# Kernel tuning notes

Hardware: AMD Instinct MI355X
Metric: run time of the kernel (lower is better)

Reference implementation:

```python
import jax, jax.numpy as jnp
import numpy as np

VOCAB, D, S, T, B, E, C = 21128, 768, 50, 5, 512, 128, 10


def gcn(x, edges, W, b):
    # GCNConv with self-loops and symmetric normalization. x: [S, D]
    N = x.shape[0]
    loop = jnp.arange(N)
    src = jnp.concatenate([edges[0], loop])
    dst = jnp.concatenate([edges[1], loop])
    deg = jax.ops.segment_sum(jnp.ones_like(src, dtype=x.dtype), dst, num_segments=N)
    dinv = jax.lax.rsqrt(jnp.maximum(deg, 1e-12))
    norm = dinv[src] * dinv[dst]
    h = x @ W  # [S, 10]
    out = jax.ops.segment_sum(h[src] * norm[:, None], dst, num_segments=N)
    return out + b


def mpm(self_f, cross_f, assign, W1, b1, W2, b2):
    # multi-perspective matching, broadcast over leading dims; node dim = -2
    a = assign * self_f
    c = assign * cross_f
    num = jnp.sum(a * c, axis=-1)
    den = jnp.maximum(jnp.linalg.norm(a, axis=-1) * jnp.linalg.norm(c, axis=-1), 1e-8)
    cos = num / den
    bshape = jnp.broadcast_shapes(self_f.shape[:-2], cross_f.shape[:-2])
    sf = jnp.broadcast_to(self_f, bshape + self_f.shape[-2:])
    h = jnp.concatenate([cos[..., None], sf], axis=-1)  # [..., S, 11]
    h = jax.nn.relu(h @ W1 + b1) @ W2 + b2  # [..., S, 20]
    return jnp.max(h, axis=-2)  # [..., 20]


def setup_inputs() -> dict:
    key = jax.random.key(0)
    ks = jax.random.split(key, 20)
    inp = {
        "context_input": jax.random.randint(ks[0], (B, T, S), 0, VOCAB),
        "response_input": jax.random.randint(ks[1], (B, S), 0, VOCAB),
        "context_graph_adjs": jax.random.randint(ks[2], (B, T, 2, E), 0, S),
        "response_graph_adj": jax.random.randint(ks[3], (B, 2, E), 0, S),
        "word_emb": jax.random.normal(ks[4], (VOCAB, D), jnp.float32) * 0.02,
        "conv_W": jax.random.normal(ks[5], (D, C), jnp.float32) * 0.05,
        "conv_b": jnp.zeros((C,), jnp.float32),
        "cross_w": jax.random.uniform(ks[6], (D, C), jnp.float32),
        "attention_coef": jax.random.uniform(ks[7], (S, S), jnp.float32),
        "assign_weight": jax.random.uniform(ks[8], (S, C), jnp.float32),
        "mp_W1": jax.random.normal(ks[9], (C + 1, 20), jnp.float32) * 0.3,
        "mp_b1": jnp.zeros((20,), jnp.float32),
        "mp_W2": jax.random.normal(ks[10], (20, 20), jnp.float32) * 0.2,
        "mp_b2": jnp.zeros((20,), jnp.float32),
        "ffn_W1": jax.random.normal(ks[11], (80, 40), jnp.float32) * 0.1,
        "ffn_b1": jnp.zeros((40,), jnp.float32),
        "ffn_W2": jax.random.normal(ks[12], (40, 1), jnp.float32) * 0.2,
        "ffn_b2": jnp.zeros((1,), jnp.float32),
    }
    return inp


def reference(context_input, response_input, context_graph_adjs, response_graph_adj,
              word_emb, conv_W, conv_b, cross_w, attention_coef, assign_weight,
              mp_W1, mp_b1, mp_W2, mp_b2, ffn_W1, ffn_b1, ffn_W2, ffn_b2):
    ctx = word_emb[context_input]      # [B, T, S, D]
    resp = word_emb[response_input]    # [B, S, D]

    gcn_b = jax.vmap(gcn, in_axes=(0, 0, None, None))
    resp_gcn = gcn_b(resp, response_graph_adj, conv_W, conv_b)                      # [B, S, C]
    ctx_gcn = jax.vmap(gcn_b, in_axes=(0, 0, None, None))(ctx, context_graph_adjs, conv_W, conv_b)  # [B, T, S, C]

    # cross features: utterance cross comes from response, response cross from utterance
    u_cross = jnp.einsum('ps,bsk->bpk', attention_coef, resp @ cross_w)   # [B, S, C]
    r_cross = jnp.einsum('ps,btsk->btpk', attention_coef, ctx @ cross_w)  # [B, T, S, C]

    g_u = mpm(ctx_gcn, u_cross[:, None], assign_weight, mp_W1, mp_b1, mp_W2, mp_b2)       # [B, T, 20]
    g_r = mpm(resp_gcn[:, None], r_cross, assign_weight, mp_W1, mp_b1, mp_W2, mp_b2)      # [B, T, 20]

    feat = jnp.concatenate([g_u, g_r, g_u * g_r, jnp.abs(g_u - g_r)], axis=-1)  # [B, T, 80]
    logits = jax.nn.relu(feat @ ffn_W1 + ffn_b1) @ ffn_W2 + ffn_b2              # [B, T, 1]
    return jax.nn.sigmoid(jnp.sum(logits, axis=1))                              # [B, 1]
```

## Files before the change

kernel.cpp:

```cpp
#include <hip/hip_runtime.h>
#include <math.h>

#define VOCAB 21128
#define DD 768
#define SS 50
#define TT 5
#define BB 512
#define EE 128
#define CC 10
#define V20 (VOCAB * 20)
#define NG 2560
#define NALL 3072

__global__ __launch_bounds__(512) void k_vocab(const float* __restrict__ emb,
                                               const float* __restrict__ Wconv,
                                               const float* __restrict__ Wcross,
                                               const float* __restrict__ att,
                                               float* __restrict__ attG,
                                               float* __restrict__ hvp) {
    __shared__ float tile[8][64][21];
    const int wv = threadIdx.x >> 6, lane = threadIdx.x & 63;
    const int rowbase = blockIdx.x * 64;

    if (rowbase >= VOCAB) {
        if (blockIdx.y == 0) {
            for (int i = threadIdx.x; i < SS * SS; i += 512) {
                int p = i / SS, s = i - p * SS;
                attG[s * 52 + p] = att[i];
            }
        }
        return;
    }

    const int rsub = lane >> 2, m = lane & 3;
    const int d0w = blockIdx.y * 384 + __builtin_amdgcn_readfirstlane(wv * 48);

    float4 v[12];
#pragma unroll
    for (int ch = 0; ch < 3; ++ch) {
#pragma unroll
        for (int it = 0; it < 4; ++it) {
            int row = it * 16 + rsub;
            long r = rowbase + row;
            if (r >= VOCAB) r = VOCAB - 1;
            v[ch * 4 + it] = *(const float4*)(emb + r * DD + d0w + ch * 16 + m * 4);
        }
    }

    float acc[20];
#pragma unroll
    for (int c = 0; c < 20; c++) acc[c] = 0.f;

#pragma unroll
    for (int ch = 0; ch < 3; ++ch) {
        const int d0 = d0w + ch * 16;
#pragma unroll
        for (int it = 0; it < 4; ++it) {
            const int row = it * 16 + rsub;
            const float4 w = v[ch * 4 + it];
            tile[wv][row][m * 4 + 0] = w.x;
            tile[wv][row][m * 4 + 1] = w.y;
            tile[wv][row][m * 4 + 2] = w.z;
            tile[wv][row][m * 4 + 3] = w.w;
        }
#pragma unroll
        for (int d = 0; d < 16; ++d) {
            float e = tile[wv][lane][d];
            const float* wc = Wconv + (d0 + d) * 10;
            const float* wx = Wcross + (d0 + d) * 10;
#pragma unroll
            for (int c = 0; c < 10; c++) {
                acc[c] = fmaf(e, wc[c], acc[c]);
                acc[10 + c] = fmaf(e, wx[c], acc[10 + c]);
            }
        }
    }

    __syncthreads();
    float* pp = &tile[0][0][0];
#pragma unroll
    for (int c = 0; c < 20; c++) pp[wv * 1280 + lane * 20 + c] = acc[c];
    __syncthreads();
    float* outp = hvp + (long)blockIdx.y * V20;
    for (int i = threadIdx.x; i < 1280; i += 512) {
        int row = i / 20;
        long r = rowbase + row;
        if (r < VOCAB) {
            float s = 0.f;
#pragma unroll
            for (int w = 0; w < 8; ++w) s += pp[w * 1280 + i];
            outp[r * 20 + (i - row * 20)] = s;
        }
    }
}

__global__ __launch_bounds__(256) void k_gcn(const int* __restrict__ ctok,
                                             const int* __restrict__ cadj,
                                             const int* __restrict__ rtok,
                                             const int* __restrict__ radj,
                                             const float* __restrict__ hvp,
                                             const float* __restrict__ convb,
                                             const float* __restrict__ attG,
                                             float* __restrict__ P) {
    __shared__ float hcv[4][SS][12];
    __shared__ float aggL[4][SS][11];
    __shared__ int dgS[4][64];
    const int tid = threadIdx.x, wv = tid >> 6, lane = tid & 63;
    const int G = blockIdx.x * 4 + wv;

    const int* tb;
    const int* ab;
    if (G < NG) { tb = ctok + (long)G * SS; ab = cadj + (long)G * 2 * EE; }
    else        { int b = G - NG; tb = rtok + (long)b * SS; ab = radj + (long)b * 2 * EE; }

    const int e1s = ab[lane], e2s = ab[lane + 64];
    const int e1d = ab[EE + lane], e2d = ab[EE + lane + 64];

    const int p = lane;
    const int pc = (p < SS) ? p : (SS - 1);
    const long t = tb[pc];
    const float4* hv4 = (const float4*)hvp;

    float4 qa[5], qb[5];
#pragma unroll
    for (int qi = 0; qi < 5; ++qi) {
        qa[qi] = hv4[t * 5 + qi];
        qb[qi] = hv4[(long)(VOCAB * 5) + t * 5 + qi];
    }
    float rowv[CC], xo[CC];
    rowv[0] = qa[0].x + qb[0].x; rowv[1] = qa[0].y + qb[0].y;
    rowv[2] = qa[0].z + qb[0].z; rowv[3] = qa[0].w + qb[0].w;
    rowv[4] = qa[1].x + qb[1].x; rowv[5] = qa[1].y + qb[1].y;
    rowv[6] = qa[1].z + qb[1].z; rowv[7] = qa[1].w + qb[1].w;
    rowv[8] = qa[2].x + qb[2].x; rowv[9] = qa[2].y + qb[2].y;
    xo[0] = qa[2].z + qb[2].z; xo[1] = qa[2].w + qb[2].w;
    xo[2] = qa[3].x + qb[3].x; xo[3] = qa[3].y + qb[3].y;
    xo[4] = qa[3].z + qb[3].z; xo[5] = qa[3].w + qb[3].w;
    xo[6] = qa[4].x + qb[4].x; xo[7] = qa[4].y + qb[4].y;
    xo[8] = qa[4].z + qb[4].z; xo[9] = qa[4].w + qb[4].w;

    dgS[wv][lane] = 0;
    atomicAdd(&dgS[wv][e1d], 1);
    atomicAdd(&dgS[wv][e2d], 1);

    if (p < SS) {
        *(float4*)&hcv[wv][p][0] = make_float4(rowv[0], rowv[1], rowv[2], rowv[3]);
        *(float4*)&hcv[wv][p][4] = make_float4(rowv[4], rowv[5], rowv[6], rowv[7]);
        *(float2*)&hcv[wv][p][8] = make_float2(rowv[8], rowv[9]);
    }

    float dv = 0.f;
    if (lane < SS) dv = rsqrtf((float)(dgS[wv][lane] + 1));

    float* aggW = &aggL[wv][0][0];
    for (int i = lane; i < SS * 11; i += 64) aggW[i] = 0.f;
    const float n1 = __shfl(dv, e1s) * __shfl(dv, e1d);
    const float n2 = __shfl(dv, e2s) * __shfl(dv, e2d);
#pragma unroll
    for (int c = 0; c < CC; c++) atomicAdd(&aggW[e1d * 11 + c], hcv[wv][e1s][c] * n1);
#pragma unroll
    for (int c = 0; c < CC; c++) atomicAdd(&aggW[e2d * 11 + c], hcv[wv][e2s][c] * n2);

    if (p < SS) {
        float gcn[CC];
        const float dp2 = dv * dv;
#pragma unroll
        for (int c = 0; c < CC; c++) gcn[c] = aggW[p * 11 + c] + rowv[c] * dp2 + convb[c];

        float ax[CC];
#pragma unroll
        for (int c = 0; c < CC; c++) ax[c] = 0.f;
#pragma unroll 5
        for (int s = 0; s < SS; ++s) {
            const float a = attG[s * 52 + p];
#pragma unroll
            for (int c = 0; c < CC; c++) {
                const float xs = __uint_as_float(
                    __builtin_amdgcn_readlane(__float_as_uint(xo[c]), s));
                ax[c] = fmaf(a, xs, ax[c]);
            }
        }
        float4* o4 = (float4*)(P + (long)G * 1000 + p * 20);
        o4[0] = make_float4(gcn[0], gcn[1], gcn[2], gcn[3]);
        o4[1] = make_float4(gcn[4], gcn[5], gcn[6], gcn[7]);
        o4[2] = make_float4(gcn[8], gcn[9], ax[0], ax[1]);
        o4[3] = make_float4(ax[2], ax[3], ax[4], ax[5]);
        o4[4] = make_float4(ax[6], ax[7], ax[8], ax[9]);
    }
}

__global__ __launch_bounds__(640) void k_mpmf(const float* __restrict__ P,
                                              const float* __restrict__ assign,
                                              const float* __restrict__ W1, const float* __restrict__ b1,
                                              const float* __restrict__ W2, const float* __restrict__ b2,
                                              const float* __restrict__ fW1, const float* __restrict__ fb1,
                                              const float* __restrict__ fW2, const float* __restrict__ fb2,
                                              float* __restrict__ out) {
    __shared__ float W2T[20][21];
    __shared__ float asgL[SS][11];
    __shared__ float h1L[10][SS][20];
    __shared__ float guS[TT][20];
    __shared__ float grS[TT][20];
    __shared__ float fsum[256];
    const int tid = threadIdx.x, wv = tid >> 6, lane = tid & 63;
    const int b = blockIdx.x;
    const int t = wv >> 1, which = wv & 1;
    const int g = b * TT + t;

    for (int i = tid; i < 400; i += 640) W2T[i % 20][i / 20] = W2[i];
    for (int i = tid; i < SS * CC; i += 640) asgL[i / CC][i % CC] = assign[i];
    __syncthreads();

    const float* Pc = P + (long)g * 1000;
    const float* Pr = P + (long)(NG + b) * 1000;
    const float* selfP = which ? Pr : Pc;
    const float* croP  = which ? Pc : Pr;

    const int p = lane;
    float self[CC], cro[CC];
    if (p < SS) {
        const float4* s4 = (const float4*)(selfP + p * 20);
        const float4 a0 = s4[0], a1 = s4[1], a2 = s4[2];
        self[0] = a0.x; self[1] = a0.y; self[2] = a0.z; self[3] = a0.w;
        self[4] = a1.x; self[5] = a1.y; self[6] = a1.z; self[7] = a1.w;
        self[8] = a2.x; self[9] = a2.y;
        const float4* c4 = (const float4*)(croP + p * 20);
        const float4 b0 = c4[2], b1q = c4[3], b2q = c4[4];
        cro[0] = b0.z; cro[1] = b0.w;
        cro[2] = b1q.x; cro[3] = b1q.y; cro[4] = b1q.z; cro[5] = b1q.w;
        cro[6] = b2q.x; cro[7] = b2q.y; cro[8] = b2q.z; cro[9] = b2q.w;
    }

    const int j = lane % 20;
    const int grp = lane / 20;
    float w2r[20];
#pragma unroll
    for (int k = 0; k < 20; k++) w2r[k] = W2T[j][k];

    if (p < SS) {
        float num = 0.f, na = 0.f, nc2 = 0.f;
#pragma unroll
        for (int c = 0; c < CC; c++) {
            float av = asgL[p][c];
            float a = av * self[c];
            float cx = av * cro[c];
            num = fmaf(a, cx, num);
            na = fmaf(a, a, na);
            nc2 = fmaf(cx, cx, nc2);
        }
        float cosv = num / fmaxf(sqrtf(na) * sqrtf(nc2), 1e-8f);
        float h1[20];
#pragma unroll
        for (int q = 0; q < 20; q++) h1[q] = fmaf(cosv, W1[q], b1[q]);
#pragma unroll
        for (int k = 0; k < CC; k++) {
            float sv = self[k];
#pragma unroll
            for (int q = 0; q < 20; q++) h1[q] = fmaf(sv, W1[(k + 1) * 20 + q], h1[q]);
        }
        float4* hw = (float4*)&h1L[wv][p][0];
        hw[0] = make_float4(fmaxf(h1[0], 0.f), fmaxf(h1[1], 0.f), fmaxf(h1[2], 0.f), fmaxf(h1[3], 0.f));
        hw[1] = make_float4(fmaxf(h1[4], 0.f), fmaxf(h1[5], 0.f), fmaxf(h1[6], 0.f), fmaxf(h1[7], 0.f));
        hw[2] = make_float4(fmaxf(h1[8], 0.f), fmaxf(h1[9], 0.f), fmaxf(h1[10], 0.f), fmaxf(h1[11], 0.f));
        hw[3] = make_float4(fmaxf(h1[12], 0.f), fmaxf(h1[13], 0.f), fmaxf(h1[14], 0.f), fmaxf(h1[15], 0.f));
        hw[4] = make_float4(fmaxf(h1[16], 0.f), fmaxf(h1[17], 0.f), fmaxf(h1[18], 0.f), fmaxf(h1[19], 0.f));
    }

    float part = -1e30f;
    if (grp < 3) {
        const int s0 = grp * 17;
        const int s1 = (grp == 2) ? SS : (s0 + 17);
        for (int s = s0; s < s1; ++s) {
            const float* hr = &h1L[wv][s][0];
            float tt = 0.f;
#pragma unroll
            for (int k = 0; k < 20; k++) tt = fmaf(hr[k], w2r[k], tt);
            part = fmaxf(part, tt);
        }
    }
    const float a0 = __shfl(part, j);
    const float a1 = __shfl(part, j + 20);
    const float a2 = __shfl(part, j + 40);
    if (lane < 20) {
        float h2 = fmaxf(fmaxf(a0, a1), a2) + b2[lane];
        (which ? grS[t] : guS[t])[lane] = h2;
    }
    __syncthreads();

    float term = 0.f;
    if (tid < 200) {
        const int tt = tid / 40, jj = tid - tt * 40;
        float hvv = fb1[jj];
#pragma unroll
        for (int k = 0; k < 20; k++) {
            float u = guS[tt][k], r = grS[tt][k];
            hvv = fmaf(u, fW1[k * 40 + jj], hvv);
            hvv = fmaf(r, fW1[(20 + k) * 40 + jj], hvv);
            hvv = fmaf(u * r, fW1[(40 + k) * 40 + jj], hvv);
            hvv = fmaf(fabsf(u - r), fW1[(60 + k) * 40 + jj], hvv);
        }
        term = fmaxf(hvv, 0.f) * fW2[jj];
    }
    if (tid < 256) fsum[tid] = term;
    __syncthreads();
    if (wv == 0) {
        float s = fsum[lane] + fsum[lane + 64] + fsum[lane + 128] + fsum[lane + 192];
#pragma unroll
        for (int o = 32; o; o >>= 1) s += __shfl_xor(s, o);
        if (lane == 0) out[b] = 1.f / (1.f + expf(-(s + (float)TT * fb2[0])));
    }
}

extern "C" void kernel_launch(void* const* d_in, const int* in_sizes, int n_in,
                              void* d_out, int out_size, void* d_ws, size_t ws_size,
                              hipStream_t stream) {
    (void)in_sizes; (void)n_in; (void)out_size; (void)ws_size;
    const int* ctx_tok = (const int*)d_in[0];
    const int* resp_tok = (const int*)d_in[1];
    const int* ctx_adj = (const int*)d_in[2];
    const int* resp_adj = (const int*)d_in[3];
    const float* emb = (const float*)d_in[4];
    const float* convW = (const float*)d_in[5];
    const float* convb = (const float*)d_in[6];
    const float* crossW = (const float*)d_in[7];
    const float* att = (const float*)d_in[8];
    const float* assign = (const float*)d_in[9];
    const float* mpW1 = (const float*)d_in[10];
    const float* mpb1 = (const float*)d_in[11];
    const float* mpW2 = (const float*)d_in[12];
    const float* mpb2 = (const float*)d_in[13];
    const float* fW1 = (const float*)d_in[14];
    const float* fb1 = (const float*)d_in[15];
    const float* fW2 = (const float*)d_in[16];
    const float* fb2 = (const float*)d_in[17];

    float* ws = (float*)d_ws;
    float* hvp = ws;
    float* P = hvp + 2 * V20;
    float* attG = P + (long)NALL * 1000;
    float* outf = (float*)d_out;

    hipLaunchKernelGGL(k_vocab, dim3((VOCAB + 63) / 64 + 1, 2), dim3(512), 0, stream,
                       emb, convW, crossW, att, attG, hvp);
    hipLaunchKernelGGL(k_gcn, dim3(NALL / 4), dim3(256), 0, stream,
                       ctx_tok, ctx_adj, resp_tok, resp_adj, hvp, convb, attG, P);
    hipLaunchKernelGGL(k_mpmf, dim3(BB), dim3(640), 0, stream,
                       P, assign, mpW1, mpb1, mpW2, mpb2, fW1, fb1, fW2, fb2, outf);
}
```

Measured before the change: 69.60 us.

## Fuse GCN and matching kernels into one per-batch kernel with LDS handoff

Merges the GCN/cross-attention kernel into the matching+FFN kernel so each block computes the six graphs of one batch (5 contexts + response) in waves 0-5 and passes them through shared memory. This removes the global round-trip of the P buffer and one kernel launch, and avoids recomputing nothing extra since the response graph is now computed once per batch. It also replaces the LDS-staged second MLP layer with per-lane register accumulation and a wave-wide shuffle max reduction. In exchange, only 6 of 10 waves do GCN work before a barrier, and the per-lane 20x20 register matmul raises register pressure.

```diff
diff --git a/kernel.cpp b/kernel.cpp
--- a/kernel.cpp
+++ b/kernel.cpp
@@ -10,7 +10,6 @@
 #define CC 10
 #define V20 (VOCAB * 20)
 #define NG 2560
-#define NALL 3072
 
 __global__ __launch_bounds__(512) void k_vocab(const float* __restrict__ emb,
                                                const float* __restrict__ Wconv,
@@ -94,154 +93,128 @@
     }
 }
 
-__global__ __launch_bounds__(256) void k_gcn(const int* __restrict__ ctok,
-                                             const int* __restrict__ cadj,
-                                             const int* __restrict__ rtok,
-                                             const int* __restrict__ radj,
-                                             const float* __restrict__ hvp,
-                                             const float* __restrict__ convb,
-                                             const float* __restrict__ attG,
-                                             float* __restrict__ P) {
-    __shared__ float hcv[4][SS][12];
-    __shared__ float aggL[4][SS][11];
-    __shared__ int dgS[4][64];
-    const int tid = threadIdx.x, wv = tid >> 6, lane = tid & 63;
-    const int G = blockIdx.x * 4 + wv;
-
-    const int* tb;
-    const int* ab;
-    if (G < NG) { tb = ctok + (long)G * SS; ab = cadj + (long)G * 2 * EE; }
-    else        { int b = G - NG; tb = rtok + (long)b * SS; ab = radj + (long)b * 2 * EE; }
-
-    const int e1s = ab[lane], e2s = ab[lane + 64];
-    const int e1d = ab[EE + lane], e2d = ab[EE + lane + 64];
-
-    const int p = lane;
-    const int pc = (p < SS) ? p : (SS - 1);
-    const long t = tb[pc];
-    const float4* hv4 = (const float4*)hvp;
-
-    float4 qa[5], qb[5];
-#pragma unroll
-    for (int qi = 0; qi < 5; ++qi) {
-        qa[qi] = hv4[t * 5 + qi];
-        qb[qi] = hv4[(long)(VOCAB * 5) + t * 5 + qi];
-    }
-    float rowv[CC], xo[CC];
-    rowv[0] = qa[0].x + qb[0].x; rowv[1] = qa[0].y + qb[0].y;
-    rowv[2] = qa[0].z + qb[0].z; rowv[3] = qa[0].w + qb[0].w;
-    rowv[4] = qa[1].x + qb[1].x; rowv[5] = qa[1].y + qb[1].y;
-    rowv[6] = qa[1].z + qb[1].z; rowv[7] = qa[1].w + qb[1].w;
-    rowv[8] = qa[2].x + qb[2].x; rowv[9] = qa[2].y + qb[2].y;
-    xo[0] = qa[2].z + qb[2].z; xo[1] = qa[2].w + qb[2].w;
-    xo[2] = qa[3].x + qb[3].x; xo[3] = qa[3].y + qb[3].y;
-    xo[4] = qa[3].z + qb[3].z; xo[5] = qa[3].w + qb[3].w;
-    xo[6] = qa[4].x + qb[4].x; xo[7] = qa[4].y + qb[4].y;
-    xo[8] = qa[4].z + qb[4].z; xo[9] = qa[4].w + qb[4].w;
-
-    dgS[wv][lane] = 0;
-    atomicAdd(&dgS[wv][e1d], 1);
-    atomicAdd(&dgS[wv][e2d], 1);
-
-    if (p < SS) {
-        *(float4*)&hcv[wv][p][0] = make_float4(rowv[0], rowv[1], rowv[2], rowv[3]);
-        *(float4*)&hcv[wv][p][4] = make_float4(rowv[4], rowv[5], rowv[6], rowv[7]);
-        *(float2*)&hcv[wv][p][8] = make_float2(rowv[8], rowv[9]);
-    }
-
-    float dv = 0.f;
-    if (lane < SS) dv = rsqrtf((float)(dgS[wv][lane] + 1));
-
-    float* aggW = &aggL[wv][0][0];
-    for (int i = lane; i < SS * 11; i += 64) aggW[i] = 0.f;
-    const float n1 = __shfl(dv, e1s) * __shfl(dv, e1d);
-    const float n2 = __shfl(dv, e2s) * __shfl(dv, e2d);
-#pragma unroll
-    for (int c = 0; c < CC; c++) atomicAdd(&aggW[e1d * 11 + c], hcv[wv][e1s][c] * n1);
-#pragma unroll
-    for (int c = 0; c < CC; c++) atomicAdd(&aggW[e2d * 11 + c], hcv[wv][e2s][c] * n2);
-
-    if (p < SS) {
-        float gcn[CC];
-        const float dp2 = dv * dv;
-#pragma unroll
-        for (int c = 0; c < CC; c++) gcn[c] = aggW[p * 11 + c] + rowv[c] * dp2 + convb[c];
-
-        float ax[CC];
-#pragma unroll
-        for (int c = 0; c < CC; c++) ax[c] = 0.f;
-#pragma unroll 5
-        for (int s = 0; s < SS; ++s) {
-            const float a = attG[s * 52 + p];
-#pragma unroll
-            for (int c = 0; c < CC; c++) {
-                const float xs = __uint_as_float(
-                    __builtin_amdgcn_readlane(__float_as_uint(xo[c]), s));
-                ax[c] = fmaf(a, xs, ax[c]);
-            }
-        }
-        float4* o4 = (float4*)(P + (long)G * 1000 + p * 20);
-        o4[0] = make_float4(gcn[0], gcn[1], gcn[2], gcn[3]);
-        o4[1] = make_float4(gcn[4], gcn[5], gcn[6], gcn[7]);
-        o4[2] = make_float4(gcn[8], gcn[9], ax[0], ax[1]);
-        o4[3] = make_float4(ax[2], ax[3], ax[4], ax[5]);
-        o4[4] = make_float4(ax[6], ax[7], ax[8], ax[9]);
-    }
-}
-
-__global__ __launch_bounds__(640) void k_mpmf(const float* __restrict__ P,
-                                              const float* __restrict__ assign,
-                                              const float* __restrict__ W1, const float* __restrict__ b1,
-                                              const float* __restrict__ W2, const float* __restrict__ b2,
-                                              const float* __restrict__ fW1, const float* __restrict__ fb1,
-                                              const float* __restrict__ fW2, const float* __restrict__ fb2,
-                                              float* __restrict__ out) {
-    __shared__ float W2T[20][21];
+__global__ __launch_bounds__(640) void k_fused(const int* __restrict__ ctok,
+                                               const int* __restrict__ cadj,
+                                               const int* __restrict__ rtok,
+                                               const int* __restrict__ radj,
+                                               const float* __restrict__ hvp,
+                                               const float* __restrict__ convb,
+                                               const float* __restrict__ attG,
+                                               const float* __restrict__ assign,
+                                               const float* __restrict__ W1, const float* __restrict__ b1,
+                                               const float* __restrict__ W2, const float* __restrict__ b2,
+                                               const float* __restrict__ fW1, const float* __restrict__ fb1,
+                                               const float* __restrict__ fW2, const float* __restrict__ fb2,
+                                               float* __restrict__ out) {
+    __shared__ float PL[6][SS][21];
+    __shared__ float hcv[6][SS][12];
+    __shared__ float aggL[6][SS][11];
+    __shared__ int dgS[6][64];
     __shared__ float asgL[SS][11];
-    __shared__ float h1L[10][SS][20];
     __shared__ float guS[TT][20];
     __shared__ float grS[TT][20];
     __shared__ float fsum[256];
     const int tid = threadIdx.x, wv = tid >> 6, lane = tid & 63;
     const int b = blockIdx.x;
-    const int t = wv >> 1, which = wv & 1;
-    const int g = b * TT + t;
-
-    for (int i = tid; i < 400; i += 640) W2T[i % 20][i / 20] = W2[i];
+
     for (int i = tid; i < SS * CC; i += 640) asgL[i / CC][i % CC] = assign[i];
-    __syncthreads();
-
-    const float* Pc = P + (long)g * 1000;
-    const float* Pr = P + (long)(NG + b) * 1000;
-    const float* selfP = which ? Pr : Pc;
-    const float* croP  = which ? Pc : Pr;
-
-    const int p = lane;
-    float self[CC], cro[CC];
-    if (p < SS) {
-        const float4* s4 = (const float4*)(selfP + p * 20);
-        const float4 a0 = s4[0], a1 = s4[1], a2 = s4[2];
-        self[0] = a0.x; self[1] = a0.y; self[2] = a0.z; self[3] = a0.w;
-        self[4] = a1.x; self[5] = a1.y; self[6] = a1.z; self[7] = a1.w;
-        self[8] = a2.x; self[9] = a2.y;
-        const float4* c4 = (const float4*)(croP + p * 20);
-        const float4 b0 = c4[2], b1q = c4[3], b2q = c4[4];
-        cro[0] = b0.z; cro[1] = b0.w;
-        cro[2] = b1q.x; cro[3] = b1q.y; cro[4] = b1q.z; cro[5] = b1q.w;
-        cro[6] = b2q.x; cro[7] = b2q.y; cro[8] = b2q.z; cro[9] = b2q.w;
-    }
-
-    const int j = lane % 20;
-    const int grp = lane / 20;
-    float w2r[20];
-#pragma unroll
-    for (int k = 0; k < 20; k++) w2r[k] = W2T[j][k];
-
-    if (p < SS) {
+
+    if (wv < 6) {
+        const bool isR = (wv == 5);
+        const int* tb = isR ? (rtok + (long)b * SS) : (ctok + ((long)b * TT + wv) * SS);
+        const int* ab = isR ? (radj + (long)b * 2 * EE) : (cadj + ((long)b * TT + wv) * 2 * EE);
+
+        const int e1s = ab[lane], e2s = ab[lane + 64];
+        const int e1d = ab[EE + lane], e2d = ab[EE + lane + 64];
+
+        const int p = lane;
+        const int pc = (p < SS) ? p : (SS - 1);
+        const long t = tb[pc];
+        const float4* hv4 = (const float4*)hvp;
+
+        float4 qa[5], qb[5];
+#pragma unroll
+        for (int qi = 0; qi < 5; ++qi) {
+            qa[qi] = hv4[t * 5 + qi];
+            qb[qi] = hv4[(long)(VOCAB * 5) + t * 5 + qi];
+        }
+        float rowv[CC], xo[CC];
+        rowv[0] = qa[0].x + qb[0].x; rowv[1] = qa[0].y + qb[0].y;
+        rowv[2] = qa[0].z + qb[0].z; rowv[3] = qa[0].w + qb[0].w;
+        rowv[4] = qa[1].x + qb[1].x; rowv[5] = qa[1].y + qb[1].y;
+        rowv[6] = qa[1].z + qb[1].z; rowv[7] = qa[1].w + qb[1].w;
+        rowv[8] = qa[2].x + qb[2].x; rowv[9] = qa[2].y + qb[2].y;
+        xo[0] = qa[2].z + qb[2].z; xo[1] = qa[2].w + qb[2].w;
+        xo[2] = qa[3].x + qb[3].x; xo[3] = qa[3].y + qb[3].y;
+        xo[4] = qa[3].z + qb[3].z; xo[5] = qa[3].w + qb[3].w;
+        xo[6] = qa[4].x + qb[4].x; xo[7] = qa[4].y + qb[4].y;
+        xo[8] = qa[4].z + qb[4].z; xo[9] = qa[4].w + qb[4].w;
+
+        dgS[wv][lane] = 0;
+        atomicAdd(&dgS[wv][e1d], 1);
+        atomicAdd(&dgS[wv][e2d], 1);
+
+        if (p < SS) {
+            *(float4*)&hcv[wv][p][0] = make_float4(rowv[0], rowv[1], rowv[2], rowv[3]);
+            *(float4*)&hcv[wv][p][4] = make_float4(rowv[4], rowv[5], rowv[6], rowv[7]);
+            *(float2*)&hcv[wv][p][8] = make_float2(rowv[8], rowv[9]);
+        }
+
+        float dv = 0.f;
+        if (lane < SS) dv = rsqrtf((float)(dgS[wv][lane] + 1));
+
+        float* aggW = &aggL[wv][0][0];
+        for (int i = lane; i < SS * 11; i += 64) aggW[i] = 0.f;
+        const float n1 = __shfl(dv, e1s) * __shfl(dv, e1d);
+        const float n2 = __shfl(dv, e2s) * __shfl(dv, e2d);
+#pragma unroll
+        for (int c = 0; c < CC; c++) atomicAdd(&aggW[e1d * 11 + c], hcv[wv][e1s][c] * n1);
+#pragma unroll
+        for (int c = 0; c < CC; c++) atomicAdd(&aggW[e2d * 11 + c], hcv[wv][e2s][c] * n2);
+
+        if (p < SS) {
+            const float dp2 = dv * dv;
+#pragma unroll
+            for (int c = 0; c < CC; c++)
+                PL[wv][p][c] = aggW[p * 11 + c] + rowv[c] * dp2 + convb[c];
+
+            float ax[CC];
+#pragma unroll
+            for (int c = 0; c < CC; c++) ax[c] = 0.f;
+#pragma unroll 5
+            for (int s = 0; s < SS; ++s) {
+                const float a = attG[s * 52 + p];
+#pragma unroll
+                for (int c = 0; c < CC; c++) {
+                    const float xs = __uint_as_float(
+                        __builtin_amdgcn_readlane(__float_as_uint(xo[c]), s));
+                    ax[c] = fmaf(a, xs, ax[c]);
+                }
+            }
+#pragma unroll
+            for (int c = 0; c < CC; c++) PL[wv][p][10 + c] = ax[c];
+        }
+    }
+    __syncthreads();
+
+    {
+        const int t = wv >> 1, which = wv & 1;
+        const int p = lane;
+        const int pcl = (p < SS) ? p : 0;
+        const int selfG = which ? 5 : t;
+        const int croG = which ? t : 5;
+
+        float self[CC], cro[CC];
+#pragma unroll
+        for (int c = 0; c < CC; c++) {
+            self[c] = PL[selfG][pcl][c];
+            cro[c] = PL[croG][pcl][10 + c];
+        }
+
         float num = 0.f, na = 0.f, nc2 = 0.f;
 #pragma unroll
         for (int c = 0; c < CC; c++) {
-            float av = asgL[p][c];
+            float av = asgL[pcl][c];
             float a = av * self[c];
             float cx = av * cro[c];
             num = fmaf(a, cx, num);
@@ -258,32 +231,33 @@
 #pragma unroll
             for (int q = 0; q < 20; q++) h1[q] = fmaf(sv, W1[(k + 1) * 20 + q], h1[q]);
         }
-        float4* hw = (float4*)&h1L[wv][p][0];
-        hw[0] = make_float4(fmaxf(h1[0], 0.f), fmaxf(h1[1], 0.f), fmaxf(h1[2], 0.f), fmaxf(h1[3], 0.f));
-        hw[1] = make_float4(fmaxf(h1[4], 0.f), fmaxf(h1[5], 0.f), fmaxf(h1[6], 0.f), fmaxf(h1[7], 0.f));
-        hw[2] = make_float4(fmaxf(h1[8], 0.f), fmaxf(h1[9], 0.f), fmaxf(h1[10], 0.f), fmaxf(h1[11], 0.f));
-        hw[3] = make_float4(fmaxf(h1[12], 0.f), fmaxf(h1[13], 0.f), fmaxf(h1[14], 0.f), fmaxf(h1[15], 0.f));
-        hw[4] = make_float4(fmaxf(h1[16], 0.f), fmaxf(h1[17], 0.f), fmaxf(h1[18], 0.f), fmaxf(h1[19], 0.f));
-    }
-
-    float part = -1e30f;
-    if (grp < 3) {
-        const int s0 = grp * 17;
-        const int s1 = (grp == 2) ? SS : (s0 + 17);
-        for (int s = s0; s < s1; ++s) {
-            const float* hr = &h1L[wv][s][0];
-            float tt = 0.f;
-#pragma unroll
-            for (int k = 0; k < 20; k++) tt = fmaf(hr[k], w2r[k], tt);
-            part = fmaxf(part, tt);
-        }
-    }
-    const float a0 = __shfl(part, j);
-    const float a1 = __shfl(part, j + 20);
-    const float a2 = __shfl(part, j + 40);
-    if (lane < 20) {
-        float h2 = fmaxf(fmaxf(a0, a1), a2) + b2[lane];
-        (which ? grS[t] : guS[t])[lane] = h2;
+#pragma unroll
+        for (int q = 0; q < 20; q++) h1[q] = fmaxf(h1[q], 0.f);
+
+        float vj[20];
+#pragma unroll
+        for (int j = 0; j < 20; j++) vj[j] = 0.f;
+#pragma unroll 4
+        for (int k = 0; k < 20; k++) {
+            const float hk = h1[k];
+            const float* wr = W2 + k * 20;
+#pragma unroll
+            for (int j = 0; j < 20; j++) vj[j] = fmaf(hk, wr[j], vj[j]);
+        }
+        if (p >= SS) {
+#pragma unroll
+            for (int j = 0; j < 20; j++) vj[j] = -1e30f;
+        }
+#pragma unroll
+        for (int off = 32; off; off >>= 1) {
+#pragma unroll
+            for (int j = 0; j < 20; j++) vj[j] = fmaxf(vj[j], __shfl_xor(vj[j], off));
+        }
+        if (lane == 0) {
+            float* dst = which ? grS[t] : guS[t];
+#pragma unroll
+            for (int j = 0; j < 20; j++) dst[j] = vj[j] + b2[j];
+        }
     }
     __syncthreads();
 
@@ -336,14 +310,12 @@
 
     float* ws = (float*)d_ws;
     float* hvp = ws;
-    float* P = hvp + 2 * V20;
-    float* attG = P + (long)NALL * 1000;
+    float* attG = hvp + 2 * V20;
     float* outf = (float*)d_out;
 
     hipLaunchKernelGGL(k_vocab, dim3((VOCAB + 63) / 64 + 1, 2), dim3(512), 0, stream,
                        emb, convW, crossW, att, attG, hvp);
-    hipLaunchKernelGGL(k_gcn, dim3(NALL / 4), dim3(256), 0, stream,
-                       ctx_tok, ctx_adj, resp_tok, resp_adj, hvp, convb, attG, P);
-    hipLaunchKernelGGL(k_mpmf, dim3(BB), dim3(640), 0, stream,
-                       P, assign, mpW1, mpb1, mpW2, mpb2, fW1, fb1, fW2, fb2, outf);
+    hipLaunchKernelGGL(k_fused, dim3(BB), dim3(640), 0, stream,
+                       ctx_tok, ctx_adj, resp_tok, resp_adj, hvp, convb, attG, assign,
+                       mpW1, mpb1, mpW2, mpb2, fW1, fb1, fW2, fb2, outf);
 }
```

Result: slower. 74.51 us (+7.0%).
